# Kernel optimization log

Measured on AMD Instinct MI355X. Metric: run time of the kernel, lower is better.

Reference implementation:

```python
import jax, jax.numpy as jnp
import numpy as np

N_NODES = 20000
N_EDGES = 320000
MUL = 64            # multiplicity of 0e and 1o node irreps
N_SPECIES = 5
N_BESSEL = 8
RAD_HIDDEN = 64
N_TP_W = 4 * MUL    # 4 uvu paths, 64 weights each
AVG_NEIGH = 16.0
SQ3 = np.sqrt(3.0).astype(np.float32)


def setup_inputs() -> dict:
    key = jax.random.key(0)
    ks = jax.random.split(key, 16)
    inp = {
        'node_feats': jax.random.normal(ks[0], (N_NODES, 4 * MUL), jnp.float32),
        'node_attrs': jax.random.uniform(ks[1], (N_NODES, N_SPECIES), jnp.float32),
        'edge_sh': jax.random.normal(ks[2], (N_EDGES, 4), jnp.float32),
        'senders': jax.random.randint(ks[3], (N_EDGES,), 0, N_NODES),
        'receivers': jax.random.randint(ks[4], (N_EDGES,), 0, N_NODES),
        'edge_embedded': jax.random.normal(ks[5], (N_EDGES, N_BESSEL), jnp.float32),
        # Linear on node feats (per-irrep mixing): 64x0e->64x0e, 64x1o->64x1o
        'Wl0': jax.random.normal(ks[6], (MUL, MUL), jnp.float32),
        'Wl1': jax.random.normal(ks[7], (MUL, MUL), jnp.float32),
        # radial MLP: 8 -> 64 -> 64 -> 256, no bias, scalar_mlp_std = 4.0
        'Wm1': jax.random.normal(ks[8], (N_BESSEL, RAD_HIDDEN), jnp.float32) * 4.0,
        'Wm2': jax.random.normal(ks[9], (RAD_HIDDEN, RAD_HIDDEN), jnp.float32) * 4.0,
        'Wm3': jax.random.normal(ks[10], (RAD_HIDDEN, N_TP_W), jnp.float32) * 4.0,
        # output Linear: (128x0e + 128x1o after TP) -> h_out (128x0e + 64x1o)
        'W2s': jax.random.normal(ks[11], (2 * MUL, 2 * MUL), jnp.float32),
        'W2v': jax.random.normal(ks[12], (2 * MUL, MUL), jnp.float32),
        # residual FullyConnectedTensorProduct(node_feats, node_attrs) -> h_out
        'Wr_s': jax.random.normal(ks[13], (MUL, N_SPECIES, 2 * MUL), jnp.float32),
        'Wr_v': jax.random.normal(ks[14], (MUL, N_SPECIES, MUL), jnp.float32),
    }
    return inp


def reference(node_feats, node_attrs, edge_sh, senders, receivers, edge_embedded,
              Wl0, Wl1, Wm1, Wm2, Wm3, W2s, W2v, Wr_s, Wr_v):
    N = node_feats.shape[0]
    x0 = node_feats[:, :MUL]                       # [N, 64]   0e scalars
    x1 = node_feats[:, MUL:].reshape(N, MUL, 3)    # [N, 64, 3] 1o vectors

    # --- residual FullyConnectedTensorProduct(node_feats, node_attrs) -> h_out ---
    # node_attrs are 0e scalars: paths 0e x 0e -> 0e and 1o x 0e -> 1o.
    nr = 1.0 / np.sqrt(MUL * N_SPECIES).astype(np.float32)  # fan-in norm
    res_s = jnp.einsum('nu,ns,usv->nv', x0, node_attrs, Wr_s) * nr   # [N, 128]
    res_v = jnp.einsum('num,ns,usv->nvm', x1, node_attrs, Wr_v) * nr # [N, 64, 3]

    # --- Linear(node_feats.irreps) ---
    nl = 1.0 / np.sqrt(MUL).astype(np.float32)
    y0 = (x0 @ Wl0) * nl                                  # [N, 64]
    y1 = jnp.einsum('num,uv->nvm', x1, Wl1) * nl          # [N, 64, 3]

    # --- gather to edges ---
    e0 = y0[senders]          # [E, 64]
    e1 = y1[senders]          # [E, 64, 3]
    sh0 = edge_sh[:, 0]       # [E]
    sh1 = edge_sh[:, 1:4]     # [E, 3]

    # --- radial MLP producing per-edge TP weights ---
    h = jax.nn.swish(edge_embedded @ Wm1 / np.sqrt(N_BESSEL, dtype=np.float32))
    h = jax.nn.swish(h @ Wm2 / np.sqrt(RAD_HIDDEN, dtype=np.float32))
    w = h @ Wm3 / np.sqrt(RAD_HIDDEN, dtype=np.float32)   # [E, 256]
    w1, w2, w3, w4 = (w[:, :MUL], w[:, MUL:2*MUL], w[:, 2*MUL:3*MUL], w[:, 3*MUL:])

    # --- equivariant tensor product (uvu), 4 paths ---
    # 0e x 0e -> 0e ; 1o x 1o -> 0e (CG = delta/sqrt(3))
    tp_s = jnp.concatenate([
        w1 * e0 * sh0[:, None],
        w4 * jnp.einsum('eum,em->eu', e1, sh1) / SQ3,
    ], axis=1)  # [E, 128]
    # 0e x 1o -> 1o ; 1o x 0e -> 1o
    tp_v = jnp.concatenate([
        w2[:, :, None] * e0[:, :, None] * sh1[:, None, :],
        w3[:, :, None] * e1 * sh0[:, None, None],
    ], axis=1)  # [E, 128, 3]

    # --- scatter-sum aggregation over receivers ---
    agg_s = jax.ops.segment_sum(tp_s, receivers, num_segments=N) / AVG_NEIGH          # [N, 128]
    agg_v = jax.ops.segment_sum(tp_v.reshape(-1, 2 * MUL * 3), receivers,
                                num_segments=N).reshape(N, 2 * MUL, 3) / AVG_NEIGH    # [N, 128, 3]

    # --- Linear(h_out_irreps) ---
    n2 = 1.0 / np.sqrt(2 * MUL).astype(np.float32)
    z_s = (agg_s @ W2s) * n2                               # [N, 128] (64 scalars + 64 gates)
    z_v = jnp.einsum('num,uv->nvm', agg_v, W2v) * n2       # [N, 64, 3]

    # residual connection
    z_s = z_s + res_s
    z_v = z_v + res_v

    # --- gate: even_act = swish on scalars and gate scalars; gated 1o vectors ---
    out_s = jax.nn.swish(z_s[:, :MUL])                     # [N, 64]
    gates = jax.nn.swish(z_s[:, MUL:])                     # [N, 64]
    out_v = gates[:, :, None] * z_v                        # [N, 64, 3]

    return jnp.concatenate([out_s, out_v.reshape(N, MUL * 3)], axis=1)  # [N, 256]
```

## Files before the change

### kernel.cpp

```cpp
#include <hip/hip_runtime.h>
#include <hip/hip_fp16.h>


#define NN 20000
#define NE 320000

typedef _Float16 h2v __attribute__((ext_vector_type(2)));
typedef _Float16 f16x8 __attribute__((ext_vector_type(8)));
typedef float f32x4 __attribute__((ext_vector_type(4)));

__device__ __forceinline__ float swishf(float x) {
  float t = __expf(-fabsf(x));
  float r = 1.0f / (1.0f + t);
  float sig = (x >= 0.0f) ? r : t * r;
  return x * sig;
}

__device__ __forceinline__ unsigned pack2h(float a, float b) {
  __half2 h = __floats2half2_rn(a, b);
  return *reinterpret_cast<unsigned*>(&h);
}

__device__ __forceinline__ h2v u32h2(unsigned u) {
  union { unsigned u; h2v h; } x; x.u = u; return x.h;
}

__device__ __forceinline__ h2v packh2v(float a, float b) {
  h2v h; h.x = (_Float16)a; h.y = (_Float16)b; return h;
}

__device__ __forceinline__ f16x8 u4f16(uint4 u) {
  union { uint4 u; f16x8 h; } x; x.u = u; return x.h;
}

__device__ __forceinline__ void ld8(float d[8], const float* p) {
  float4 a0 = *(const float4*)p;
  float4 a1 = *(const float4*)(p + 4);
  d[0]=a0.x; d[1]=a0.y; d[2]=a0.z; d[3]=a0.w;
  d[4]=a1.x; d[5]=a1.y; d[6]=a1.z; d[7]=a1.w;
}

__device__ __forceinline__ void fma8v(float (&acc)[8], const float* p, float w) {
  float4 a0 = *(const float4*)p;
  float4 a1 = *(const float4*)(p + 4);
  acc[0] = fmaf(a0.x, w, acc[0]); acc[1] = fmaf(a0.y, w, acc[1]);
  acc[2] = fmaf(a0.z, w, acc[2]); acc[3] = fmaf(a0.w, w, acc[3]);
  acc[4] = fmaf(a1.x, w, acc[4]); acc[5] = fmaf(a1.y, w, acc[5]);
  acc[6] = fmaf(a1.z, w, acc[6]); acc[7] = fmaf(a1.w, w, acc[7]);
}

__global__ __launch_bounds__(256) void hist_kernel(const int* __restrict__ rcv,
                                                   int* __restrict__ counts) {
  int e = blockIdx.x * 256 + threadIdx.x;
  atomicAdd(&counts[rcv[e]], 1);
}

__global__ __launch_bounds__(1024) void scan_kernel(const int* __restrict__ counts,
                                                    int* __restrict__ offsets,
                                                    int* __restrict__ cursor) {
  __shared__ int part[1024];
  const int t = threadIdx.x;
  const int base = t * 20;
  int loc[20];
  int s = 0;
  #pragma unroll
  for (int j = 0; j < 20; ++j) {
    int idx = base + j;
    int c = (idx < NN) ? counts[idx] : 0;
    loc[j] = s;
    s += c;
  }
  part[t] = s;
  __syncthreads();
  for (int d = 1; d < 1024; d <<= 1) {
    int v = (t >= d) ? part[t - d] : 0;
    __syncthreads();
    part[t] += v;
    __syncthreads();
  }
  int excl = (t > 0) ? part[t - 1] : 0;
  #pragma unroll
  for (int j = 0; j < 20; ++j) {
    int idx = base + j;
    if (idx < NN) {
      int o = excl + loc[j];
      offsets[idx] = o;
      cursor[idx] = o;
    }
  }
  if (t == 1023) offsets[NN] = part[1023];
}

__global__ __launch_bounds__(256) void scatter_full(
    const int* __restrict__ rcv, const int* __restrict__ snd,
    const float* __restrict__ esh, int* __restrict__ cursor,
    int* __restrict__ csr_edge, int* __restrict__ snd_sorted,
    float* __restrict__ sh_sorted) {
  int e = blockIdx.x * 256 + threadIdx.x;
  int r = rcv[e];
  int pos = atomicAdd(&cursor[r], 1);
  csr_edge[pos] = e;
  snd_sorted[pos] = snd[e];
  float4 sh = *(const float4*)(esh + (size_t)e * 4);
  *(float4*)(sh_sorted + (size_t)pos * 4) = sh;
}

__global__ __launch_bounds__(256) void scatter_kernel(
    const int* __restrict__ rcv, int* __restrict__ cursor,
    int* __restrict__ csr_edge) {
  int e = blockIdx.x * 256 + threadIdx.x;
  int r = rcv[e];
  int pos = atomicAdd(&cursor[r], 1);
  csr_edge[pos] = e;
}

__global__ __launch_bounds__(256) void pack_weights(
    const float* __restrict__ Wm2, const float* __restrict__ Wm3,
    unsigned* __restrict__ Wm2P, unsigned* __restrict__ Wm3P,
    unsigned* __restrict__ Wm3T) {
  int idx = blockIdx.x * 256 + threadIdx.x;
  if (idx < 2048) {
    int k2 = idx >> 6, v = idx & 63;
    Wm2P[idx] = pack2h(Wm2[(2 * k2) * 64 + v], Wm2[(2 * k2 + 1) * 64 + v]);
  } else if (idx < 10240) {
    int r = idx - 2048;
    int k2 = r >> 8, c = r & 255;
    Wm3P[r] = pack2h(Wm3[(2 * k2) * 256 + c], Wm3[(2 * k2 + 1) * 256 + c]);
  } else if (idx < 18432) {
    int r = idx - 10240;
    int c = r >> 5, j = r & 31;
    Wm3T[r] = pack2h(Wm3[(2 * j) * 256 + c], Wm3[(2 * j + 1) * 256 + c]);
  }
}

__global__ __launch_bounds__(256) void pack_node_B(
    const float* __restrict__ Wr_s, const float* __restrict__ W2s,
    const float* __restrict__ Wr_v, const float* __restrict__ W2v,
    unsigned* __restrict__ BsT, unsigned* __restrict__ BvT) {
  const float nr = 0.05590169943749474f;
  const float n2 = 0.08838834764831845f;
  int idx = blockIdx.x * 256 + threadIdx.x;
  if (idx < 28672) {
    int v = idx / 224, j = idx % 224;
    float a, b;
    if (j < 160) {
      int s = j >> 5, u0 = (j & 31) << 1;
      a = Wr_s[(u0 * 5 + s) * 128 + v] * nr;
      b = Wr_s[((u0 + 1) * 5 + s) * 128 + v] * nr;
    } else {
      int c0 = (j - 160) << 1;
      a = W2s[c0 * 128 + v] * n2;
      b = W2s[(c0 + 1) * 128 + v] * n2;
    }
    BsT[idx] = pack2h(a, b);
  } else if (idx < 43008) {
    int r = idx - 28672;
    int v = r / 224, j = r % 224;
    float a, b;
    if (j < 160) {
      int s = j >> 5, u0 = (j & 31) << 1;
      a = Wr_v[(u0 * 5 + s) * 64 + v] * nr;
      b = Wr_v[((u0 + 1) * 5 + s) * 64 + v] * nr;
    } else {
      int c0 = (j - 160) << 1;
      a = W2v[c0 * 64 + v] * n2;
      b = W2v[(c0 + 1) * 64 + v] * n2;
    }
    BvT[r] = pack2h(a, b);
  }
}

__global__ __launch_bounds__(256) void node_prep(
    const float* __restrict__ feats, const float* __restrict__ Wl0,
    const float* __restrict__ Wl1, float* __restrict__ y)
{
  __shared__ __align__(16) float sX[4 * 256];
  const int t = threadIdx.x;
  const int n0 = blockIdx.x * 4;
  #pragma unroll
  for (int nb = 0; nb < 4; ++nb)
    sX[nb * 256 + t] = feats[(size_t)(n0 + nb) * 256 + t];
  __syncthreads();

  float acc[4] = {0.f, 0.f, 0.f, 0.f};
  if (t < 64) {
    const int v = t;
    for (int u = 0; u < 64; ++u) {
      float w = Wl0[u * 64 + v];
      acc[0] = fmaf(sX[0 * 256 + u], w, acc[0]);
      acc[1] = fmaf(sX[1 * 256 + u], w, acc[1]);
      acc[2] = fmaf(sX[2 * 256 + u], w, acc[2]);
      acc[3] = fmaf(sX[3 * 256 + u], w, acc[3]);
    }
  } else {
    const int i = t - 64;
    const int v = i / 3;
    const int m = i - v * 3;
    for (int u = 0; u < 64; ++u) {
      float w = Wl1[u * 64 + v];
      int xi = 64 + u * 3 + m;
      acc[0] = fmaf(sX[0 * 256 + xi], w, acc[0]);
      acc[1] = fmaf(sX[1 * 256 + xi], w, acc[1]);
      acc[2] = fmaf(sX[2 * 256 + xi], w, acc[2]);
      acc[3] = fmaf(sX[3 * 256 + xi], w, acc[3]);
    }
  }
  #pragma unroll
  for (int nb = 0; nb < 4; ++nb)
    y[(size_t)(n0 + nb) * 256 + t] = acc[nb] * 0.125f;
}

__device__ __forceinline__ void wgemv(float (&wa)[64], const float* __restrict__ Wm3,
                                      const float* h2col, int p)
{
  #pragma unroll
  for (int v = 0; v < 64; ++v) wa[v] = 0.f;
  #pragma unroll 2
  for (int k = 0; k < 64; ++k) {
    float h2k = h2col[k * 256];
    const float* wrow = Wm3 + k * 256 + p * 64;
    #pragma unroll
    for (int v = 0; v < 64; ++v) wa[v] = fmaf(h2k, wrow[v], wa[v]);
  }
}

__global__ __launch_bounds__(256, 4) void w_kernel(
    const int* __restrict__ csr_edge, const float* __restrict__ emb,
    const float* __restrict__ Wm1, const unsigned* __restrict__ Wm2P,
    const unsigned* __restrict__ Wm3T, __half* __restrict__ w_sorted)
{
  __shared__ unsigned sA[256 * 32];
  const int tid = threadIdx.x;
  const int i = blockIdx.x * 256 + tid;
  const int e = csr_edge[i];

  float e8[8];
  ld8(e8, emb + (size_t)e * 8);
  float h2a[64];
  #pragma unroll
  for (int v = 0; v < 64; ++v) h2a[v] = 0.f;
  #pragma unroll 1
  for (int k2 = 0; k2 < 32; ++k2) {
    float a0 = 0.f, a1 = 0.f;
    #pragma unroll
    for (int j = 0; j < 8; ++j) {
      a0 = fmaf(e8[j], Wm1[j * 64 + 2 * k2], a0);
      a1 = fmaf(e8[j], Wm1[j * 64 + 2 * k2 + 1], a1);
    }
    h2v ph = packh2v(swishf(a0 * 0.35355339059327373f),
                     swishf(a1 * 0.35355339059327373f));
    const unsigned* wrow = Wm2P + k2 * 64;
    #pragma unroll
    for (int v = 0; v < 64; ++v)
      h2a[v] = __builtin_amdgcn_fdot2(ph, u32h2(wrow[v]), h2a[v], false);
  }
  {
    const int r = tid;
    #pragma unroll
    for (int c = 0; c < 8; ++c) {
      uint4 v;
      v.x = pack2h(swishf(h2a[8 * c + 0] * 0.125f), swishf(h2a[8 * c + 1] * 0.125f));
      v.y = pack2h(swishf(h2a[8 * c + 2] * 0.125f), swishf(h2a[8 * c + 3] * 0.125f));
      v.z = pack2h(swishf(h2a[8 * c + 4] * 0.125f), swishf(h2a[8 * c + 5] * 0.125f));
      v.w = pack2h(swishf(h2a[8 * c + 6] * 0.125f), swishf(h2a[8 * c + 7] * 0.125f));
      *(uint4*)&sA[r * 32 + ((c ^ (r & 7)) << 2)] = v;
    }
  }
  __syncthreads();

  const int l = tid & 63;
  const int wv = tid >> 6;
  const int lg = l >> 4;
  const int lm = l & 15;

  f16x8 bfr[4][2];
  #pragma unroll
  for (int nt = 0; nt < 4; ++nt) {
    int row = wv * 64 + nt * 16 + lm;
    #pragma unroll
    for (int kh = 0; kh < 2; ++kh) {
      uint4 u = *(const uint4*)&sA[row * 32 + ((((kh << 2) + lg) ^ (row & 7)) << 2)];
      bfr[nt][kh] = u4f16(u);
    }
  }
  unsigned* sTw = sA + wv * 2048;
  const int eb = blockIdx.x * 256 + wv * 64;

  #pragma unroll 1
  for (int p = 0; p < 4; ++p) {
    #pragma unroll
    for (int mtl = 0; mtl < 4; ++mtl) {
      const int mt = p * 4 + mtl;
      int arow = mt * 16 + lm;
      uint4 u0 = *(const uint4*)&Wm3T[arow * 32 + (lg << 2)];
      uint4 u1 = *(const uint4*)&Wm3T[arow * 32 + 16 + (lg << 2)];
      f16x8 a0 = u4f16(u0), a1 = u4f16(u1);
      #pragma unroll
      for (int nt = 0; nt < 4; ++nt) {
        f32x4 acc = {0.f, 0.f, 0.f, 0.f};
        acc = __builtin_amdgcn_mfma_f32_16x16x32_f16(a0, bfr[nt][0], acc, 0, 0, 0);
        acc = __builtin_amdgcn_mfma_f32_16x16x32_f16(a1, bfr[nt][1], acc, 0, 0, 0);
        const int r = nt * 16 + lm;
        const int u = mtl * 4 + lg;
        const int pos8 = ((((u >> 1) ^ (r & 7)) << 1) | (u & 1));
        uint2 pk;
        pk.x = pack2h(acc[0], acc[1]);
        pk.y = pack2h(acc[2], acc[3]);
        *(uint2*)&sTw[r * 32 + pos8 * 2] = pk;
      }
    }
    #pragma unroll
    for (int g = 0; g < 8; ++g) {
      const int er = g * 8 + (l >> 3);
      const int c8 = l & 7;
      uint4 v = *(const uint4*)&sTw[er * 32 + ((c8 ^ (er & 7)) << 2)];
      *(uint4*)(w_sorted + (size_t)(eb + er) * 256 + p * 64 + c8 * 8) = v;
    }
  }
}

__global__ __launch_bounds__(256) void gather_tp(
    const float* __restrict__ y, const __half* __restrict__ w_sorted,
    const float* __restrict__ sh_sorted, const int* __restrict__ snd_sorted,
    const int* __restrict__ offsets, float* __restrict__ agg)
{
  const int l = threadIdx.x & 63;
  const int wv = threadIdx.x >> 6;
  const int n = blockIdx.x * 4 + wv;
  const int row0 = offsets[n];
  const int row1 = offsets[n + 1];

  float s0 = 0.f, s1 = 0.f;
  float v0x = 0.f, v0y = 0.f, v0z = 0.f;
  float v1x = 0.f, v1y = 0.f, v1z = 0.f;

  for (int i = row0; i < row1; ++i) {
    const int s = snd_sorted[i];
    const float4 sh = *(const float4*)(sh_sorted + (size_t)i * 4);
    const __half* wr = w_sorted + (size_t)i * 256;
    float w1 = __half2float(wr[l]);
    float w2 = __half2float(wr[64 + l]);
    float w3 = __half2float(wr[128 + l]);
    float w4 = __half2float(wr[192 + l]);
    const float* yr = y + (size_t)s * 256;
    float e0 = yr[l];
    float ex = yr[64 + 3 * l], ey = yr[65 + 3 * l], ez = yr[66 + 3 * l];

    s0 = fmaf(w1 * e0, sh.x, s0);
    s1 = fmaf(w4, fmaf(ex, sh.y, fmaf(ey, sh.z, ez * sh.w)), s1);
    float t2 = w2 * e0;
    v0x = fmaf(t2, sh.y, v0x); v0y = fmaf(t2, sh.z, v0y); v0z = fmaf(t2, sh.w, v0z);
    float t3 = w3 * sh.x;
    v1x = fmaf(t3, ex, v1x); v1y = fmaf(t3, ey, v1y); v1z = fmaf(t3, ez, v1z);
  }

  const float SCL = 0.0078125f;
  const float C4  = 0.125f / (16.0f * 1.7320508075688772f);
  float* ar = agg + (size_t)n * 512;
  ar[l]       = s0 * SCL;
  ar[64 + l]  = s1 * C4;
  ar[128 + l]        = v0x * SCL;
  ar[128 + 64 + l]   = v1x * SCL;
  ar[256 + l]        = v0y * SCL;
  ar[256 + 64 + l]   = v1y * SCL;
  ar[384 + l]        = v0z * SCL;
  ar[384 + 64 + l]   = v1z * SCL;
}

__global__ __launch_bounds__(256) void node_gemm(
    const float* __restrict__ feats, const float* __restrict__ attrs,
    const float* __restrict__ agg, const unsigned* __restrict__ BsT,
    const unsigned* __restrict__ BvT, float* __restrict__ out)
{
  __shared__ unsigned sAK[64 * 128];
  __shared__ float zsL[16 * 128];
  __shared__ __half zvL[48 * 64];
  __shared__ float sAt[16 * 5];
  const int t = threadIdx.x;
  const int n0 = blockIdx.x * 16;

  if (t < 80) sAt[t] = attrs[(size_t)n0 * 5 + t];
  __syncthreads();

  const int l = t & 63;
  const int wv = t >> 6;
  const int lm = l & 15;
  const int lg = l >> 4;

  f32x4 acc[5];
  #pragma unroll
  for (int jj = 0; jj < 5; ++jj) acc[jj] = (f32x4){0.f, 0.f, 0.f, 0.f};

  #pragma unroll 1
  for (int h = 0; h < 2; ++h) {
    {
      const int row = t >> 2;
      const int part = t & 3;
      const bool is_s = row < 16;
      int node, m = 0;
      if (is_s) node = row;
      else { int vi = row - 16; node = vi / 3; m = vi - node * 3; }
      const float* xrow = feats + (size_t)(n0 + node) * 256;
      const float* atr = &sAt[node * 5];
      const float* aggr = agg + (size_t)(n0 + node) * 512;
      unsigned* arow = &sAK[row * 128];
      #pragma unroll 7
      for (int jj = 0; jj < 28; ++jj) {
        const int jl = part + 4 * jj;
        const int jg = h * 112 + jl;
        float v0, v1;
        if (jg < 160) {
          int s = jg >> 5;
          int u0 = (jg & 31) << 1;
          float a = atr[s];
          float x0 = is_s ? xrow[u0]     : xrow[64 + 3 * u0 + m];
          float x1 = is_s ? xrow[u0 + 1] : xrow[64 + 3 * u0 + 3 + m];
          v0 = x0 * a;
          v1 = x1 * a;
        } else {
          int c0 = (jg - 160) << 1;
          if (is_s) { v0 = aggr[c0]; v1 = aggr[c0 + 1]; }
          else {
            v0 = aggr[128 + m * 128 + c0];
            v1 = aggr[128 + m * 128 + c0 + 1];
          }
        }
        int chs = (jj & ~7) | ((jj ^ row) & 7);
        arow[(chs << 2) + part] = pack2h(v0, v1);
      }
    }
    __syncthreads();

    #pragma unroll
    for (int jj = 0; jj < 5; ++jj) {
      const int jd = wv + 4 * jj;
      int mtile, ntile;
      const unsigned* Bt;
      if (jd < 8) { mtile = 0; ntile = jd; Bt = BsT; }
      else { int q = jd - 8; mtile = 1 + (q >> 2); ntile = q & 3; Bt = BvT; }

      const int arow0 = mtile * 16 + lm;
      const unsigned* brow = Bt + (ntile * 16 + lm) * 224 + h * 112;

      uint4 ubr[7];
      #pragma unroll
      for (int ks = 0; ks < 7; ++ks)
        ubr[ks] = *(const uint4*)&brow[(ks * 4 + lg) << 2];

      f32x4 a = acc[jj];
      #pragma unroll
      for (int ks = 0; ks < 7; ++ks) {
        int ch = ks * 4 + lg;
        int chs = (ch & ~7) | ((ch ^ arow0) & 7);
        uint4 ua = *(const uint4*)&sAK[arow0 * 128 + (chs << 2)];
        a = __builtin_amdgcn_mfma_f32_16x16x32_f16(u4f16(ua), u4f16(ubr[ks]), a, 0, 0, 0);
      }
      acc[jj] = a;
    }
    __syncthreads();
  }

  #pragma unroll
  for (int jj = 0; jj < 5; ++jj) {
    const int jd = wv + 4 * jj;
    int mtile, ntile;
    if (jd < 8) { mtile = 0; ntile = jd; }
    else { int q = jd - 8; mtile = 1 + (q >> 2); ntile = q & 3; }
    const int drow = mtile * 16 + lg * 4;
    if (jd < 8) {
      #pragma unroll
      for (int rr = 0; rr < 4; ++rr)
        zsL[(drow + rr) * 128 + ntile * 16 + lm] = acc[jj][rr];
    } else {
      const int vi0 = drow - 16;
      #pragma unroll
      for (int rr = 0; rr < 4; ++rr)
        zvL[(vi0 + rr) * 64 + ntile * 16 + lm] = __float2half(acc[jj][rr]);
    }
  }
  __syncthreads();

  int ug = 0, mg = 0;
  if (t >= 64) { ug = (t - 64) / 3; mg = (t - 64) - ug * 3; }
  #pragma unroll 4
  for (int nb = 0; nb < 16; ++nb) {
    float val;
    if (t < 64) {
      val = swishf(zsL[nb * 128 + t]);
    } else {
      float gate = swishf(zsL[nb * 128 + 64 + ug]);
      val = gate * __half2float(zvL[(nb * 3 + mg) * 64 + ug]);
    }
    out[(size_t)(n0 + nb) * 256 + t] = val;
  }
}

__global__ __launch_bounds__(512, 2) void gather_fused(
    const float* __restrict__ y, const int* __restrict__ csr_edge,
    const int* __restrict__ snd, const float* __restrict__ esh,
    const float* __restrict__ emb, const float* __restrict__ Wm1,
    const float* __restrict__ Wm2, const float* __restrict__ Wm3,
    const int* __restrict__ offsets, float* __restrict__ agg)
{
  __shared__ __align__(16) float sW3[64 * 256];
  __shared__ __align__(16) float sH[8 * 4 * 64];
  const int t = threadIdx.x;

  #pragma unroll 4
  for (int i = 0; i < 32; ++i) {
    int idx = i * 512 + t;
    int k = idx >> 8;
    int c = idx & 255;
    float v = Wm3[idx];
    int kg = k >> 2, kk = k & 3;
    sW3[c * 64 + (((kg ^ (c & 15)) & 15) << 2) + kk] = v;
  }
  __syncthreads();

  const int l = t & 63;
  const int wv = t >> 6;
  const int n = blockIdx.x * 8 + wv;
  const int row0 = offsets[n];
  const int row1 = offsets[n + 1];

  float* sHw = &sH[wv * 256];

  float wm1r[8];
  #pragma unroll
  for (int j = 0; j < 8; ++j) wm1r[j] = Wm1[j * 64 + l];

  float s0 = 0.f, s1 = 0.f;
  float v0x = 0.f, v0y = 0.f, v0z = 0.f;
  float v1x = 0.f, v1y = 0.f, v1z = 0.f;

  const int swz = ((l & 15) << 2);

  for (int i = row0; i < row1; i += 4) {
    const int nb = row1 - i;

    int   sn[4];
    float4 sh[4];
    #pragma unroll
    for (int b = 0; b < 4; ++b) {
      int idx = (b < nb) ? (i + b) : i;
      int e = csr_edge[idx];
      sn[b] = snd[e];
      float4 s = *(const float4*)(esh + (size_t)e * 4);
      if (b >= nb) s = make_float4(0.f, 0.f, 0.f, 0.f);
      sh[b] = s;
      float em8[8];
      ld8(em8, emb + (size_t)e * 8);
      float a = 0.f;
      #pragma unroll
      for (int j = 0; j < 8; ++j) a = fmaf(em8[j], wm1r[j], a);
      sHw[b * 64 + l] = swishf(a * 0.35355339059327373f);
    }

    float h2[4] = {0.f, 0.f, 0.f, 0.f};
    #pragma unroll 4
    for (int q = 0; q < 16; ++q) {
      float wq0 = Wm2[(4 * q + 0) * 64 + l];
      float wq1 = Wm2[(4 * q + 1) * 64 + l];
      float wq2 = Wm2[(4 * q + 2) * 64 + l];
      float wq3 = Wm2[(4 * q + 3) * 64 + l];
      #pragma unroll
      for (int b = 0; b < 4; ++b) {
        float4 h = *(const float4*)&sHw[b * 64 + 4 * q];
        h2[b] = fmaf(h.x, wq0, h2[b]);
        h2[b] = fmaf(h.y, wq1, h2[b]);
        h2[b] = fmaf(h.z, wq2, h2[b]);
        h2[b] = fmaf(h.w, wq3, h2[b]);
      }
    }
    #pragma unroll
    for (int b = 0; b < 4; ++b)
      h2[b] = swishf(h2[b] * 0.125f);
    #pragma unroll
    for (int b = 0; b < 4; ++b)
      sHw[b * 64 + l] = h2[b];

    float w0[4]  = {0,0,0,0}, w1a[4] = {0,0,0,0};
    float w2a[4] = {0,0,0,0}, w3a[4] = {0,0,0,0};
    #pragma unroll 1
    for (int g = 0; g < 16; ++g) {
      int sbase = l * 64 + (((g << 2) ^ swz) & 63);
      float4 m0 = *(const float4*)&sW3[sbase];
      float4 m1 = *(const float4*)&sW3[sbase + 4096];
      float4 m2 = *(const float4*)&sW3[sbase + 8192];
      float4 m3 = *(const float4*)&sW3[sbase + 12288];
      #pragma unroll
      for (int b = 0; b < 4; ++b) {
        float4 hb = *(const float4*)&sHw[b * 64 + 4 * g];
        #pragma unroll
        for (int kk = 0; kk < 4; ++kk) {
          float bc = (&hb.x)[kk];
          w0[b]  = fmaf(bc, (&m0.x)[kk], w0[b]);
          w1a[b] = fmaf(bc, (&m1.x)[kk], w1a[b]);
          w2a[b] = fmaf(bc, (&m2.x)[kk], w2a[b]);
          w3a[b] = fmaf(bc, (&m3.x)[kk], w3a[b]);
        }
      }
    }

    #pragma unroll
    for (int b = 0; b < 4; ++b) {
      const float* yr = y + (size_t)sn[b] * 256;
      float e0 = yr[l];
      float ex = yr[64 + 3 * l], ey = yr[65 + 3 * l], ez = yr[66 + 3 * l];
      float4 s = sh[b];
      s0 = fmaf(w0[b] * e0, s.x, s0);
      s1 = fmaf(w3a[b], fmaf(ex, s.y, fmaf(ey, s.z, ez * s.w)), s1);
      float t2 = w1a[b] * e0;
      v0x = fmaf(t2, s.y, v0x); v0y = fmaf(t2, s.z, v0y); v0z = fmaf(t2, s.w, v0z);
      float t3 = w2a[b] * s.x;
      v1x = fmaf(t3, ex, v1x); v1y = fmaf(t3, ey, v1y); v1z = fmaf(t3, ez, v1z);
    }
  }

  const float SCL = 0.0078125f;
  const float C4  = 0.125f / (16.0f * 1.7320508075688772f);
  float* ar = agg + (size_t)n * 512;
  ar[l]       = s0 * SCL;
  ar[64 + l]  = s1 * C4;
  ar[128 + 3 * l]     = v0x * SCL;
  ar[128 + 3 * l + 1] = v0y * SCL;
  ar[128 + 3 * l + 2] = v0z * SCL;
  ar[320 + 3 * l]     = v1x * SCL;
  ar[320 + 3 * l + 1] = v1y * SCL;
  ar[320 + 3 * l + 2] = v1z * SCL;
}

__global__ __launch_bounds__(256) void edge_kernel(
    const float* __restrict__ y, const float* __restrict__ edge_sh,
    const int* __restrict__ senders, const int* __restrict__ receivers,
    const float* __restrict__ emb, const float* __restrict__ Wm1,
    const float* __restrict__ Wm2, const float* __restrict__ Wm3,
    float* __restrict__ agg)
{
  __shared__ float h2s[64 * 256];
  const int tid = threadIdx.x;
  const int e = blockIdx.x * 256 + tid;
  const int s = senders[e];
  const int r = receivers[e];
  const float4 shv = *(const float4*)(edge_sh + (size_t)e * 4);
  float e8[8];
  ld8(e8, emb + (size_t)e * 8);

  float h2a[64];
  #pragma unroll
  for (int v = 0; v < 64; ++v) h2a[v] = 0.f;
  #pragma unroll 2
  for (int k = 0; k < 64; ++k) {
    float a = 0.f;
    #pragma unroll
    for (int j = 0; j < 8; ++j) a = fmaf(e8[j], Wm1[j * 64 + k], a);
    float h1k = swishf(a * 0.35355339059327373f);
    const float* wrow = Wm2 + k * 64;
    #pragma unroll
    for (int v = 0; v < 64; ++v) h2a[v] = fmaf(h1k, wrow[v], h2a[v]);
  }
  #pragma unroll
  for (int v = 0; v < 64; ++v)
    h2s[v * 256 + tid] = swishf(h2a[v] * 0.125f);

  const float* yrow = y + (size_t)s * 256;
  float* aggr = agg + (size_t)r * 512;
  const float SCL = 0.0078125f;
  const float c0  = shv.x * SCL;
  const float c1x = shv.y * SCL, c1y = shv.z * SCL, c1z = shv.w * SCL;
  const float c4  = 0.125f / (16.0f * 1.7320508075688772f);

  float wa[64];

  wgemv(wa, Wm3, h2s + tid, 0);
  #pragma unroll
  for (int uc = 0; uc < 8; ++uc) {
    float ev[8];
    ld8(ev, yrow + uc * 8);
    #pragma unroll
    for (int j = 0; j < 8; ++j) {
      int u = uc * 8 + j;
      atomicAdd(&aggr[u], wa[u] * ev[j] * c0);
    }
  }
  wgemv(wa, Wm3, h2s + tid, 1);
  #pragma unroll
  for (int uc = 0; uc < 8; ++uc) {
    float ev[8];
    ld8(ev, yrow + uc * 8);
    #pragma unroll
    for (int j = 0; j < 8; ++j) {
      int u = uc * 8 + j;
      float tt = wa[u] * ev[j];
      atomicAdd(&aggr[128 + 3 * u    ], tt * c1x);
      atomicAdd(&aggr[128 + 3 * u + 1], tt * c1y);
      atomicAdd(&aggr[128 + 3 * u + 2], tt * c1z);
    }
  }
  wgemv(wa, Wm3, h2s + tid, 2);
  #pragma unroll
  for (int uc = 0; uc < 8; ++uc) {
    float ev[24];
    ld8(ev,      yrow + 64 + uc * 24);
    ld8(ev + 8,  yrow + 64 + uc * 24 + 8);
    ld8(ev + 16, yrow + 64 + uc * 24 + 16);
    #pragma unroll
    for (int j = 0; j < 8; ++j) {
      int u = uc * 8 + j;
      float tt = wa[u] * c0;
      atomicAdd(&aggr[320 + 3 * u    ], tt * ev[3 * j    ]);
      atomicAdd(&aggr[320 + 3 * u + 1], tt * ev[3 * j + 1]);
      atomicAdd(&aggr[320 + 3 * u + 2], tt * ev[3 * j + 2]);
    }
  }
  wgemv(wa, Wm3, h2s + tid, 3);
  #pragma unroll
  for (int uc = 0; uc < 8; ++uc) {
    float ev[24];
    ld8(ev,      yrow + 64 + uc * 24);
    ld8(ev + 8,  yrow + 64 + uc * 24 + 8);
    ld8(ev + 16, yrow + 64 + uc * 24 + 16);
    #pragma unroll
    for (int j = 0; j < 8; ++j) {
      int u = uc * 8 + j;
      float d = ev[3*j]*shv.y + ev[3*j+1]*shv.z + ev[3*j+2]*shv.w;
      atomicAdd(&aggr[64 + u], wa[u] * d * c4);
    }
  }
}

__global__ __launch_bounds__(256) void node_post(
    const float* __restrict__ feats, const float* __restrict__ attrs,
    const float* __restrict__ agg, const float* __restrict__ W2s,
    const float* __restrict__ W2v, const float* __restrict__ Wr_s,
    const float* __restrict__ Wr_v, float* __restrict__ out)
{
  __shared__ __align__(16) float sA[320 * 8];
  __shared__ __align__(16) float sX0[64 * 8];
  __shared__ __align__(16) float sX1[192 * 8];
  __shared__ __align__(16) float sAt[5 * 8];
  __shared__ __align__(16) float sAggS[128 * 8];
  __shared__ __align__(16) float sAggV[384 * 8];
  __shared__ __align__(16) float sZs[8 * 128];
  __shared__ __align__(16) float sZv[8 * 192];

  const int t = threadIdx.x;
  const int n0 = blockIdx.x * 8;
  const float nr = 0.05590169943749474f;
  const float n2 = 0.08838834764831845f;

  #pragma unroll
  for (int nb = 0; nb < 8; ++nb) {
    float v = feats[(size_t)(n0 + nb) * 256 + t];
    if (t < 64) sX0[t * 8 + nb] = v;
    else        sX1[(t - 64) * 8 + nb] = v;
  }
  if (t < 40) {
    int nb = t & 7, s = t >> 3;
    sAt[s * 8 + nb] = attrs[(size_t)(n0 + nb) * 5 + s] * nr;
  }
  #pragma unroll
  for (int i = 0; i < 16; ++i) {
    int idx = i * 256 + t;
    int nb = idx >> 9;
    int c = idx & 511;
    float v = agg[(size_t)(n0 + nb) * 512 + c] * n2;
    if (c < 128) sAggS[c * 8 + nb] = v;
    else         sAggV[(c - 128) * 8 + nb] = v;
  }
  __syncthreads();

  #pragma unroll
  for (int i = 0; i < 10; ++i) {
    int idx = i * 256 + t;
    int nb = idx & 7;
    int us = idx >> 3;
    int u = us / 5;
    int s = us - u * 5;
    sA[us * 8 + nb] = sX0[u * 8 + nb] * sAt[s * 8 + nb];
  }
  __syncthreads();

  float av[8][3];

  if (t < 128) {
    const int v = t;
    float acc[8];
    #pragma unroll
    for (int nb = 0; nb < 8; ++nb) acc[nb] = 0.f;
    for (int us = 0; us < 320; ++us)
      fma8v(acc, &sA[us * 8], Wr_s[us * 128 + v]);
    for (int c = 0; c < 128; ++c)
      fma8v(acc, &sAggS[c * 8], W2s[c * 128 + v]);
    #pragma unroll
    for (int nb = 0; nb < 8; ++nb) sZs[nb * 128 + v] = acc[nb];
  } else {
    const int tv = t - 128;
    const int v = tv & 63;
    const int half = tv >> 6;
    #pragma unroll
    for (int nb = 0; nb < 8; ++nb)
      #pragma unroll
      for (int m = 0; m < 3; ++m) av[nb][m] = 0.f;

    const int u0 = half * 32;
    for (int u = u0; u < u0 + 32; ++u) {
      float xr0[8], xr1[8], xr2[8];
      ld8(xr0, &sX1[(u * 3 + 0) * 8]);
      ld8(xr1, &sX1[(u * 3 + 1) * 8]);
      ld8(xr2, &sX1[(u * 3 + 2) * 8]);
      #pragma unroll
      for (int s = 0; s < 5; ++s) {
        float w = Wr_v[(u * 5 + s) * 64 + v];
        float at[8];
        ld8(at, &sAt[s * 8]);
        #pragma unroll
        for (int nb = 0; nb < 8; ++nb) {
          float tt = at[nb] * w;
          av[nb][0] = fmaf(xr0[nb], tt, av[nb][0]);
          av[nb][1] = fmaf(xr1[nb], tt, av[nb][1]);
          av[nb][2] = fmaf(xr2[nb], tt, av[nb][2]);
        }
      }
    }
    const int c0 = half * 64;
    for (int c = c0; c < c0 + 64; ++c) {
      float w = W2v[c * 64 + v];
      float g0[8], g1[8], g2[8];
      ld8(g0, &sAggV[(c * 3 + 0) * 8]);
      ld8(g1, &sAggV[(c * 3 + 1) * 8]);
      ld8(g2, &sAggV[(c * 3 + 2) * 8]);
      #pragma unroll
      for (int nb = 0; nb < 8; ++nb) {
        av[nb][0] = fmaf(g0[nb], w, av[nb][0]);
        av[nb][1] = fmaf(g1[nb], w, av[nb][1]);
        av[nb][2] = fmaf(g2[nb], w, av[nb][2]);
      }
    }
    if (half == 0) {
      #pragma unroll
      for (int nb = 0; nb < 8; ++nb)
        #pragma unroll
        for (int m = 0; m < 3; ++m)
          sZv[nb * 192 + v * 3 + m] = av[nb][m];
    }
  }
  __syncthreads();
  if (t >= 192) {
    const int v = (t - 128) & 63;
    #pragma unroll
    for (int nb = 0; nb < 8; ++nb)
      #pragma unroll
      for (int m = 0; m < 3; ++m)
        sZv[nb * 192 + v * 3 + m] += av[nb][m];
  }
  __syncthreads();

  const int i = t - 64;
  const int ug = (t >= 64) ? (i / 3) : 0;
  #pragma unroll
  for (int nb = 0; nb < 8; ++nb) {
    float val;
    if (t < 64) {
      val = swishf(sZs[nb * 128 + t]);
    } else {
      float gate = swishf(sZs[nb * 128 + 64 + ug]);
      val = gate * sZv[nb * 192 + i];
    }
    out[(size_t)(n0 + nb) * 256 + t] = val;
  }
}

extern "C" void kernel_launch(void* const* d_in, const int* in_sizes, int n_in,
                              void* d_out, int out_size, void* d_ws, size_t ws_size,
                              hipStream_t stream)
{
  const float* feats = (const float*)d_in[0];
  const float* attrs = (const float*)d_in[1];
  const float* esh   = (const float*)d_in[2];
  const int*   snd   = (const int*)d_in[3];
  const int*   rcv   = (const int*)d_in[4];
  const float* emb   = (const float*)d_in[5];
  const float* Wl0   = (const float*)d_in[6];
  const float* Wl1   = (const float*)d_in[7];
  const float* Wm1   = (const float*)d_in[8];
  const float* Wm2   = (const float*)d_in[9];
  const float* Wm3   = (const float*)d_in[10];
  const float* W2s   = (const float*)d_in[11];
  const float* W2v   = (const float*)d_in[12];
  const float* Wr_s  = (const float*)d_in[13];
  const float* Wr_v  = (const float*)d_in[14];
  float* out = (float*)d_out;

  float* y   = (float*)d_ws;
  float* agg = y + (size_t)NN * 256;
  int* counts = (int*)agg;
  int* cursor = counts + NN;
  int* csr_edge = (int*)(agg + (size_t)NN * 512);
  int* offsets  = csr_edge + NE;
  int* snd_sorted = offsets + NN + 1;
  float* sh_sorted = (float*)(snd_sorted + NE);
  __half* w_sorted = (__half*)(sh_sorted + (size_t)NE * 4);
  unsigned* Wm2P = (unsigned*)(w_sorted + (size_t)NE * 256);
  unsigned* Wm3P = Wm2P + 2048;
  unsigned* Wm3T = Wm3P + 8192;
  unsigned* BsT  = Wm3T + 8192;
  unsigned* BvT  = BsT + 28672;
  size_t need1 = (size_t)((char*)(BvT + 14336) - (char*)d_ws);
  size_t need2 = (size_t)((char*)(offsets + NN + 1) - (char*)d_ws);

  if (ws_size >= need1) {
    hipMemsetAsync(counts, 0, (size_t)NN * sizeof(int), stream);
    hist_kernel<<<NE / 256, 256, 0, stream>>>(rcv, counts);
    scan_kernel<<<1, 1024, 0, stream>>>(counts, offsets, cursor);
    scatter_full<<<NE / 256, 256, 0, stream>>>(rcv, snd, esh, cursor,
                                               csr_edge, snd_sorted, sh_sorted);
    pack_weights<<<72, 256, 0, stream>>>(Wm2, Wm3, Wm2P, Wm3P, Wm3T);
    pack_node_B<<<168, 256, 0, stream>>>(Wr_s, W2s, Wr_v, W2v, BsT, BvT);
    node_prep<<<NN / 4, 256, 0, stream>>>(feats, Wl0, Wl1, y);
    w_kernel<<<NE / 256, 256, 0, stream>>>(csr_edge, emb, Wm1, Wm2P, Wm3T, w_sorted);
    gather_tp<<<NN / 4, 256, 0, stream>>>(y, w_sorted, sh_sorted, snd_sorted,
                                          offsets, agg);
    node_gemm<<<NN / 16, 256, 0, stream>>>(feats, attrs, agg, BsT, BvT, out);
  } else if (ws_size >= need2) {
    hipMemsetAsync(counts, 0, (size_t)NN * sizeof(int), stream);
    hist_kernel<<<NE / 256, 256, 0, stream>>>(rcv, counts);
    scan_kernel<<<1, 1024, 0, stream>>>(counts, offsets, cursor);
    scatter_kernel<<<NE / 256, 256, 0, stream>>>(rcv, cursor, csr_edge);
    node_prep<<<NN / 4, 256, 0, stream>>>(feats, Wl0, Wl1, y);
    gather_fused<<<NN / 8, 512, 0, stream>>>(y, csr_edge, snd, esh, emb,
                                             Wm1, Wm2, Wm3, offsets, agg);
    node_post<<<NN / 8, 256, 0, stream>>>(feats, attrs, agg, W2s, W2v, Wr_s, Wr_v, out);
  } else {
    hipMemsetAsync(agg, 0, (size_t)NN * 512 * sizeof(float), stream);
    node_prep<<<NN / 4, 256, 0, stream>>>(feats, Wl0, Wl1, y);
    edge_kernel<<<NE / 256, 256, 0, stream>>>(y, esh, snd, rcv, emb, Wm1, Wm2, Wm3, agg);
    node_post<<<NN / 8, 256, 0, stream>>>(feats, attrs, agg, W2s, W2v, Wr_s, Wr_v, out);
  }
}
```

Before: 337.5 us.

## Prefetch second K-half global loads into registers during first MFMA phase

The node-update kernel now splits staging of the A tile into separate global-load and LDS-store steps. The second half's feature and aggregate values are loaded into 56 registers before the first MFMA phase runs, which overlaps global-memory latency with matrix math. The cost is higher register pressure, which may lower occupancy or cause spills.

```diff
diff --git a/kernel.cpp b/kernel.cpp
--- a/kernel.cpp
+++ b/kernel.cpp
@@ -387,50 +387,22 @@
   const int lm = l & 15;
   const int lg = l >> 4;
 
+  const int row = t >> 2;
+  const int part = t & 3;
+  const bool is_s = row < 16;
+  int node, m = 0;
+  if (is_s) node = row;
+  else { int vi = row - 16; node = vi / 3; m = vi - node * 3; }
+  const float* xrow = feats + (size_t)(n0 + node) * 256;
+  const float* atr = &sAt[node * 5];
+  const float* aggr = agg + (size_t)(n0 + node) * 512;
+  unsigned* arow = &sAK[row * 128];
+
   f32x4 acc[5];
   #pragma unroll
   for (int jj = 0; jj < 5; ++jj) acc[jj] = (f32x4){0.f, 0.f, 0.f, 0.f};
 
-  #pragma unroll 1
-  for (int h = 0; h < 2; ++h) {
-    {
-      const int row = t >> 2;
-      const int part = t & 3;
-      const bool is_s = row < 16;
-      int node, m = 0;
-      if (is_s) node = row;
-      else { int vi = row - 16; node = vi / 3; m = vi - node * 3; }
-      const float* xrow = feats + (size_t)(n0 + node) * 256;
-      const float* atr = &sAt[node * 5];
-      const float* aggr = agg + (size_t)(n0 + node) * 512;
-      unsigned* arow = &sAK[row * 128];
-      #pragma unroll 7
-      for (int jj = 0; jj < 28; ++jj) {
-        const int jl = part + 4 * jj;
-        const int jg = h * 112 + jl;
-        float v0, v1;
-        if (jg < 160) {
-          int s = jg >> 5;
-          int u0 = (jg & 31) << 1;
-          float a = atr[s];
-          float x0 = is_s ? xrow[u0]     : xrow[64 + 3 * u0 + m];
-          float x1 = is_s ? xrow[u0 + 1] : xrow[64 + 3 * u0 + 3 + m];
-          v0 = x0 * a;
-          v1 = x1 * a;
-        } else {
-          int c0 = (jg - 160) << 1;
-          if (is_s) { v0 = aggr[c0]; v1 = aggr[c0 + 1]; }
-          else {
-            v0 = aggr[128 + m * 128 + c0];
-            v1 = aggr[128 + m * 128 + c0 + 1];
-          }
-        }
-        int chs = (jj & ~7) | ((jj ^ row) & 7);
-        arow[(chs << 2) + part] = pack2h(v0, v1);
-      }
-    }
-    __syncthreads();
-
+  auto mfma_phase = [&](int h) {
     #pragma unroll
     for (int jj = 0; jj < 5; ++jj) {
       const int jd = wv + 4 * jj;
@@ -457,8 +429,60 @@
       }
       acc[jj] = a;
     }
-    __syncthreads();
-  }
+  };
+
+  float r0[28], r1[28];
+
+  #pragma unroll
+  for (int jj = 0; jj < 28; ++jj) {
+    const int jg = part + 4 * jj;
+    int u0 = (jg & 31) << 1;
+    if (is_s) { r0[jj] = xrow[u0];              r1[jj] = xrow[u0 + 1]; }
+    else      { r0[jj] = xrow[64 + 3 * u0 + m]; r1[jj] = xrow[64 + 3 * u0 + 3 + m]; }
+  }
+
+  #pragma unroll
+  for (int jj = 0; jj < 28; ++jj) {
+    const int jg = part + 4 * jj;
+    float a = atr[jg >> 5];
+    int chs = (jj & ~7) | ((jj ^ row) & 7);
+    arow[(chs << 2) + part] = pack2h(r0[jj] * a, r1[jj] * a);
+  }
+  __syncthreads();
+
+  #pragma unroll
+  for (int jj = 0; jj < 28; ++jj) {
+    const int jg = 112 + part + 4 * jj;
+    if (jj < 12) {
+      int u0 = (jg & 31) << 1;
+      if (is_s) { r0[jj] = xrow[u0];              r1[jj] = xrow[u0 + 1]; }
+      else      { r0[jj] = xrow[64 + 3 * u0 + m]; r1[jj] = xrow[64 + 3 * u0 + 3 + m]; }
+    } else {
+      int c0 = (jg - 160) << 1;
+      if (is_s) { r0[jj] = aggr[c0];                  r1[jj] = aggr[c0 + 1]; }
+      else      { r0[jj] = aggr[128 + m * 128 + c0];  r1[jj] = aggr[128 + m * 128 + c0 + 1]; }
+    }
+  }
+
+  mfma_phase(0);
+  __syncthreads();
+
+  #pragma unroll
+  for (int jj = 0; jj < 28; ++jj) {
+    const int jg = 112 + part + 4 * jj;
+    float v0, v1;
+    if (jj < 12) {
+      float a = atr[jg >> 5];
+      v0 = r0[jj] * a; v1 = r1[jj] * a;
+    } else {
+      v0 = r0[jj]; v1 = r1[jj];
+    }
+    int chs = (jj & ~7) | ((jj ^ row) & 7);
+    arow[(chs << 2) + part] = pack2h(v0, v1);
+  }
+  __syncthreads();
+
+  mfma_phase(1);
 
   #pragma unroll
   for (int jj = 0; jj < 5; ++jj) {
```

After: 332.5 us. No clear change (-1.5%).
